# Optimization experiments

Measured on AMD Instinct MI355X. Metric: run time of the kernel, lower is better.

Reference implementation:

```python
import jax, jax.numpy as jnp
import numpy as np
from jax import lax

TOP_N = 4
CAT_NUM = 4
IOU_THRESH = 0.25
PAD = 224
OUT_SZ = 224


def _gen_edge_anchors():
    # Faithful port of NTSNet._generate_default_anchor_maps for 448x448 input.
    settings = (
        dict(stride=32, size=48, scale=[2 ** (1.0 / 3.0), 2 ** (2.0 / 3.0)], ar=[0.667, 1, 1.5]),
        dict(stride=64, size=96, scale=[2 ** (1.0 / 3.0), 2 ** (2.0 / 3.0)], ar=[0.667, 1, 1.5]),
        dict(stride=128, size=192, scale=[1, 2 ** (1.0 / 3.0), 2 ** (2.0 / 3.0)], ar=[0.667, 1, 1.5]),
    )
    inp = np.array([448, 448], dtype=np.float32)
    edges = []
    for s in settings:
        stride = s['stride']
        oh, ow = np.ceil(inp / stride).astype(int)
        ostart = stride / 2.0
        oy = np.arange(ostart, ostart + stride * oh, stride, dtype=np.float32).reshape(oh, 1)
        ox = np.arange(ostart, ostart + stride * ow, stride, dtype=np.float32).reshape(1, ow)
        cy = np.broadcast_to(oy, (oh, ow)); cx = np.broadcast_to(ox, (oh, ow))
        for sc in s['scale']:
            for ar in s['ar']:
                h = s['size'] * sc / float(ar) ** 0.5
                w = s['size'] * sc * float(ar) ** 0.5
                e = np.stack([cy - h / 2.0, cx - w / 2.0, cy + h / 2.0, cx + w / 2.0], axis=-1).reshape(-1, 4)
                edges.append(e)
    return np.concatenate(edges, 0).astype(np.float32)

EDGE_ANCHORS = (_gen_edge_anchors() + PAD).astype(np.int32)  # [1614,4] (y0,x0,y1,x1) in padded coords
BOXES_F = jnp.asarray(EDGE_ANCHORS, jnp.float32)
BOXES_I = jnp.asarray(EDGE_ANCHORS, jnp.int32)
AREAS = (BOXES_F[:, 2] - BOXES_F[:, 0]) * (BOXES_F[:, 3] - BOXES_F[:, 1])
N_ANCHORS = EDGE_ANCHORS.shape[0]  # 1614


def _nms_single(scores):
    # Greedy hard NMS: pick top score, suppress IoU >= thresh, repeat TOP_N times.
    def step(valid, _):
        s = jnp.where(valid, scores, -jnp.inf)
        i = jnp.argmax(s)
        b = BOXES_F[i]
        sy = jnp.maximum(BOXES_F[:, 0], b[0]); sx = jnp.maximum(BOXES_F[:, 1], b[1])
        ey = jnp.minimum(BOXES_F[:, 2], b[2]); ex = jnp.minimum(BOXES_F[:, 3], b[3])
        ly = ey - sy; lx = ex - sx
        inter = jnp.where((ly < 0) | (lx < 0), 0.0, ly * lx)
        iou = inter / (AREAS + AREAS[i] - inter)
        return valid & (iou < IOU_THRESH), i
    _, idx = lax.scan(step, jnp.ones((N_ANCHORS,), bool), None, length=TOP_N)
    return idx  # [TOP_N] int


def _crop_resize(img, box):
    # img: [3, 896, 896]; box: int [4] = (y0,x0,y1,x1); bilinear, align_corners=True -> [3,224,224]
    hmax = img.shape[-1] - 1
    y0, x0, y1, x1 = box[0], box[1], box[2], box[3]
    t = jnp.arange(OUT_SZ, dtype=jnp.float32) / (OUT_SZ - 1.0)
    ys = y0.astype(jnp.float32) + t * (y1 - y0 - 1).astype(jnp.float32)
    xs = x0.astype(jnp.float32) + t * (x1 - x0 - 1).astype(jnp.float32)
    yf = jnp.floor(ys); xf = jnp.floor(xs)
    wy = (ys - yf)[None, :, None]; wx = (xs - xf)[None, None, :]
    yl = yf.astype(jnp.int32); yh = jnp.minimum(yl + 1, hmax)
    xl = xf.astype(jnp.int32); xh = jnp.minimum(xl + 1, hmax)
    g = lambda yi, xi: img[:, yi[:, None], xi[None, :]]
    top = g(yl, xl) * (1.0 - wx) + g(yl, xh) * wx
    bot = g(yh, xl) * (1.0 - wx) + g(yh, xh) * wx
    return top * (1.0 - wy) + bot * wy


def _conv(x, w, b, stride, pad):
    y = lax.conv_general_dilated(x, w, (stride, stride), ((pad, pad), (pad, pad)),
                                 dimension_numbers=('NCHW', 'OIHW', 'NCHW'))
    return y + b[None, :, None, None]


def _forward(x, bb_w, bb_b, w1, b1, t1w, t1b, w2, b2, t2w, t2b, w3, b3, t3w, t3b, cw, cb):
    B = x.shape[0]
    backbone = lambda z: jax.nn.relu(_conv(z, bb_w, bb_b, 32, 0))
    raw_pre = backbone(x)  # [B,2048,14,14]
    # Navigator unit
    y1 = jax.nn.relu(_conv(raw_pre, w1, b1, 1, 1))                                  # [B,128,14,14]
    z1 = (jnp.einsum('bchw,oc->bohw', y1, t1w) + t1b[None, :, None, None]).reshape(B, -1)
    y2 = jax.nn.relu(_conv(y1, w2, b2, 2, 1))                                        # [B,128,7,7]
    z2 = (jnp.einsum('bchw,oc->bohw', y2, t2w) + t2b[None, :, None, None]).reshape(B, -1)
    y3 = jax.nn.relu(_conv(y2, w3, b3, 2, 1))                                        # [B,128,4,4]
    z3 = (jnp.einsum('bchw,oc->bohw', y3, t3w) + t3b[None, :, None, None]).reshape(B, -1)
    rpn_score = jnp.concatenate([z1, z2, z3], axis=1)  # [B,1614]
    top_idx = jax.vmap(_nms_single)(rpn_score)          # [B,TOP_N]
    boxes = BOXES_I[top_idx]                            # [B,TOP_N,4]
    x_pad = jnp.pad(x, ((0, 0), (0, 0), (PAD, PAD), (PAD, PAD)))  # [B,3,896,896]
    parts = jax.vmap(lambda img, bs: jax.vmap(lambda b: _crop_resize(img, b))(bs))(x_pad, boxes)
    parts = lax.stop_gradient(parts).reshape(B * TOP_N, 3, OUT_SZ, OUT_SZ)  # .detach() in torch
    part_feat = backbone(parts).mean(axis=(2, 3)).reshape(B, TOP_N, 2048)
    part_feat = part_feat[:, :CAT_NUM].reshape(B, -1)   # [B,8192]
    raw_feat = lax.stop_gradient(raw_pre).mean(axis=(2, 3))  # [B,2048] (detached in torch)
    concat = jnp.concatenate([part_feat, raw_feat], axis=1)  # [B,10240]
    return concat @ cw.T + cb                           # [B,200]


def setup_inputs() -> dict:
    key = jax.random.key(0)
    ks = jax.random.split(key, 12)
    def w(k, shape, fan_in):
        return jax.random.normal(k, shape, jnp.float32) * np.float32(np.sqrt(2.0 / fan_in))
    return {
        'x': jax.random.normal(ks[0], (8, 3, 448, 448), jnp.float32),
        'bb_w': w(ks[1], (2048, 3, 32, 32), 3 * 32 * 32), 'bb_b': jnp.zeros((2048,), jnp.float32),
        'w1': w(ks[2], (128, 2048, 3, 3), 2048 * 9), 'b1': jnp.zeros((128,), jnp.float32),
        't1w': w(ks[3], (6, 128), 128), 't1b': jnp.zeros((6,), jnp.float32),
        'w2': w(ks[4], (128, 128, 3, 3), 128 * 9), 'b2': jnp.zeros((128,), jnp.float32),
        't2w': w(ks[5], (6, 128), 128), 't2b': jnp.zeros((6,), jnp.float32),
        'w3': w(ks[6], (128, 128, 3, 3), 128 * 9), 'b3': jnp.zeros((128,), jnp.float32),
        't3w': w(ks[7], (9, 128), 128), 't3b': jnp.zeros((9,), jnp.float32),
        'cw': w(ks[8], (200, 2048 * (CAT_NUM + 1)), 2048 * (CAT_NUM + 1)),
        'cb': jnp.zeros((200,), jnp.float32),
    }


def reference(x, bb_w, bb_b, w1, b1, t1w, t1b, w2, b2, t2w, t2b, w3, b3, t3w, t3b, cw, cb):
    return _forward(x, bb_w, bb_b, w1, b1, t1w, t1b, w2, b2, t2w, t2b, w3, b3, t3w, t3b, cw, cb)
```

## Files before the change

### kernel.cpp

```cpp
#include <hip/hip_runtime.h>
#include <math.h>


typedef _Float16 h8 __attribute__((ext_vector_type(8)));
typedef float f32x4 __attribute__((ext_vector_type(4)));

#define ASCALE 256.0f
#define WSCALE 16384.0f
#define RSCALE (1.0f / (256.0f * 16384.0f))
#define PSLAB ((size_t)1664 * 2048)

__device__ __forceinline__ void gload16(const void* g, void* l) {
  __builtin_amdgcn_global_load_lds(
      (__attribute__((address_space(1))) void*)(void*)(uintptr_t)g,
      (__attribute__((address_space(3))) void*)l, 16, 0, 0);
}

__device__ void anchors_body(int i, int* anch, float* areas) {
  if (i >= 1614) return;
  int stride, oh, a, pos;
  double size, sc;
  const double C13 = 1.2599210498948732;
  const double C23 = 1.5874010519681994;
  if (i < 1176) {
    stride = 32; size = 48.0; oh = 14; a = i / 196; pos = i % 196;
    sc = (a / 3 == 0) ? C13 : C23;
  } else if (i < 1470) {
    int r = i - 1176; stride = 64; size = 96.0; oh = 7; a = r / 49; pos = r % 49;
    sc = (a / 3 == 0) ? C13 : C23;
  } else {
    int r = i - 1470; stride = 128; size = 192.0; oh = 4; a = r / 16; pos = r % 16;
    int si = a / 3;
    sc = (si == 0) ? 1.0 : ((si == 1) ? C13 : C23);
  }
  int ari = a % 3;
  double ar = (ari == 0) ? 0.667 : ((ari == 1) ? 1.0 : 1.5);
  int gy = pos / oh, gx = pos % oh;
  float cy = 0.5f * (float)stride + (float)(stride * gy);
  float cx = 0.5f * (float)stride + (float)(stride * gx);
  double ss = sqrt(ar);
  double hd = (size * sc) / ss;
  double wd = (size * sc) * ss;
  float hh = (float)(hd * 0.5), wh = (float)(wd * 0.5);
  int y0 = (int)((cy - hh) + 224.0f), x0 = (int)((cx - wh) + 224.0f);
  int y1i = (int)((cy + hh) + 224.0f), x1i = (int)((cx + wh) + 224.0f);
  anch[i * 4 + 0] = y0; anch[i * 4 + 1] = x0;
  anch[i * 4 + 2] = y1i; anch[i * 4 + 3] = x1i;
  areas[i] = (float)(y1i - y0) * (float)(x1i - x0);
}

__global__ __launch_bounds__(256) void prep_small(int* __restrict__ anch,
                                                  float* __restrict__ areas,
                                                  const float* __restrict__ w2,
                                                  float* __restrict__ w2p,
                                                  const float* __restrict__ w3,
                                                  float* __restrict__ w3p) {
  int b = blockIdx.x, t = threadIdx.x;
  if (b < 7) { anchors_body(b * 256 + t, anch, areas); return; }
  const float* src; float* dst; int idx;
  if (b < 7 + 576) { src = w2; dst = w2p; idx = (b - 7) * 256 + t; }
  else             { src = w3; dst = w3p; idx = (b - 583) * 256 + t; }
  if (idx >= 128 * 9 * 128) return;
  int c = idx % 128; int r2 = idx / 128; int tap = r2 % 9; int o = r2 / 9;
  dst[idx] = src[(o * 128 + c) * 9 + tap];
}

__global__ __launch_bounds__(256) void split_w(const float* __restrict__ src,
                                               _Float16* __restrict__ h,
                                               _Float16* __restrict__ l, int n8) {
  int i = blockIdx.x * 256 + threadIdx.x;
  if (i >= n8) return;
  float4 v0 = *(const float4*)(src + (size_t)i * 8);
  float4 v1 = *(const float4*)(src + (size_t)i * 8 + 4);
  float vv[8] = {v0.x, v0.y, v0.z, v0.w, v1.x, v1.y, v1.z, v1.w};
  h8 vh, vl;
#pragma unroll
  for (int j = 0; j < 8; ++j) {
    float s = vv[j] * WSCALE;
    _Float16 a = (_Float16)s;
    vh[j] = a; vl[j] = (_Float16)(s - (float)a);
  }
  *(h8*)(h + (size_t)i * 8) = vh;
  *(h8*)(l + (size_t)i * 8) = vl;
}

__global__ __launch_bounds__(256) void split_w1(const float* __restrict__ w1,
                                                _Float16* __restrict__ h,
                                                _Float16* __restrict__ l) {
  int idx = blockIdx.x * 256 + threadIdx.x;
  if (idx >= 128 * 9 * 2048) return;
  int c = idx & 2047; int rest = idx >> 11; int tap = rest % 9; int o = rest / 9;
  float v = w1[(o * 2048 + c) * 9 + tap] * WSCALE;
  _Float16 a = (_Float16)v;
  h[idx] = a; l[idx] = (_Float16)(v - (float)a);
}

__global__ __launch_bounds__(256) void split_x(const float* __restrict__ x,
                                               _Float16* __restrict__ Ah,
                                               _Float16* __restrict__ Al) {
  int i = blockIdx.x * 256 + threadIdx.x;
  if (i >= 1664 * 384) return;
  int kq = i % 384, m = i / 384;
  int k = kq * 8;
  h8 vh = {}, vl = {};
  if (m < 1568) {
    int b = m / 196, pos = m % 196;
    int c = k >> 10, r = (k >> 5) & 31, col = k & 31;
    int py = (pos / 14) * 32 + r, px = (pos % 14) * 32 + col;
    const float* sp2 = x + (((size_t)(b * 3 + c) * 448 + py) * 448 + px);
    float4 v0 = *(const float4*)sp2;
    float4 v1 = *(const float4*)(sp2 + 4);
    float vv[8] = {v0.x, v0.y, v0.z, v0.w, v1.x, v1.y, v1.z, v1.w};
#pragma unroll
    for (int j = 0; j < 8; ++j) {
      float s = vv[j] * ASCALE;
      _Float16 a = (_Float16)s;
      vh[j] = a; vl[j] = (_Float16)(s - (float)a);
    }
  }
  *(h8*)(Ah + (size_t)m * 3072 + k) = vh;
  *(h8*)(Al + (size_t)m * 3072 + k) = vl;
}

__global__ __launch_bounds__(256) void gemm_bb_mfma(
    const _Float16* __restrict__ Ah, const _Float16* __restrict__ Al,
    const _Float16* __restrict__ Bh, const _Float16* __restrict__ Bl,
    float* __restrict__ P) {
  __shared__ __align__(16) char lds[65536];
  const int t = threadIdx.x;
  const int bid = blockIdx.x + 13 * blockIdx.y;
  const int orig = (bid & 7) * 26 + (bid >> 3);
  const int m0 = (orig % 13) * 128, n0 = (orig / 13) * 128;
  const int kz = blockIdx.z;
  const int lane = t & 63, w = t >> 6;
  const int wm = (w >> 1) * 64, wn = (w & 1) * 64;
  const int lrow = lane & 15, kg = lane >> 4;

  int offA[4], offB[4];
#pragma unroll
  for (int i = 0; i < 4; ++i) {
    int ba = (wm + i * 16 + lrow) * 64 + kg * 16;
    offA[i] = ba ^ (((ba >> 7) & 3) << 4);
    int bb2 = (wn + i * 16 + lrow) * 64 + kg * 16;
    offB[i] = bb2 ^ (((bb2 >> 7) & 3) << 4);
  }
  size_t gAo[2], gBo[2];
  int ldso[2];
#pragma unroll
  for (int e = 0; e < 2; ++e) {
    int p = e * 256 + t;
    int lsl = p ^ ((p >> 3) & 3);
    int row = lsl >> 2, kq = lsl & 3;
    gAo[e] = (size_t)(m0 + row) * 3072 + kq * 8;
    gBo[e] = (size_t)(n0 + row) * 3072 + kq * 8;
    ldso[e] = e * 4096 + (t & 192) * 16;
  }

  auto STAGE = [&](int buf, int k0) {
    char* L = lds + buf * 32768;
#pragma unroll
    for (int e = 0; e < 2; ++e) {
      gload16(Ah + gAo[e] + k0, L + ldso[e]);
      gload16(Al + gAo[e] + k0, L + 8192 + ldso[e]);
      gload16(Bh + gBo[e] + k0, L + 16384 + ldso[e]);
      gload16(Bl + gBo[e] + k0, L + 24576 + ldso[e]);
    }
  };

  f32x4 acc[4][4] = {};
  const int kbeg = kz * 768, kend = kbeg + 768;
  STAGE(0, kbeg);
  __syncthreads();
  int cur = 0;
  for (int k0 = kbeg; k0 < kend; k0 += 32) {
    if (k0 + 32 < kend) STAGE(cur ^ 1, k0 + 32);
    const char* L = lds + cur * 32768;
    h8 fah[4], fal[4], fbh[4], fbl[4];
#pragma unroll
    for (int i = 0; i < 4; ++i) {
      fah[i] = *(const h8*)(L + offA[i]);
      fal[i] = *(const h8*)(L + 8192 + offA[i]);
      fbh[i] = *(const h8*)(L + 16384 + offB[i]);
      fbl[i] = *(const h8*)(L + 24576 + offB[i]);
    }
#pragma unroll
    for (int i = 0; i < 4; ++i)
#pragma unroll
      for (int j = 0; j < 4; ++j)
        acc[i][j] = __builtin_amdgcn_mfma_f32_16x16x32_f16(fah[i], fbh[j], acc[i][j], 0, 0, 0);
#pragma unroll
    for (int i = 0; i < 4; ++i)
#pragma unroll
      for (int j = 0; j < 4; ++j)
        acc[i][j] = __builtin_amdgcn_mfma_f32_16x16x32_f16(fah[i], fbl[j], acc[i][j], 0, 0, 0);
#pragma unroll
    for (int i = 0; i < 4; ++i)
#pragma unroll
      for (int j = 0; j < 4; ++j)
        acc[i][j] = __builtin_amdgcn_mfma_f32_16x16x32_f16(fal[i], fbh[j], acc[i][j], 0, 0, 0);
    __syncthreads();
    cur ^= 1;
  }
  float* Pz = P + (size_t)kz * PSLAB;
  const int prow = (lane >> 4) * 4;
#pragma unroll
  for (int i = 0; i < 4; ++i) {
#pragma unroll
    for (int j = 0; j < 4; ++j) {
      int n = n0 + wn + j * 16 + lrow;
#pragma unroll
      for (int r = 0; r < 4; ++r) {
        int m = m0 + wm + i * 16 + prow + r;
        Pz[(size_t)m * 2048 + n] = acc[i][j][r];
      }
    }
  }
}

template <int WRITE_SPLIT>
__global__ __launch_bounds__(256) void bb_reduce(const float* __restrict__ P,
                                                 const float* __restrict__ bias,
                                                 float* __restrict__ raw,
                                                 _Float16* __restrict__ h,
                                                 _Float16* __restrict__ l) {
  int idx = blockIdx.x * 256 + threadIdx.x;
  int m = idx >> 8, col = (idx & 255) * 8;
  if (WRITE_SPLIT) {
    if (m >= 1664) return;
    if (m >= 1568) {
      h8 z = {};
      *(h8*)(h + (size_t)m * 2048 + col) = z;
      *(h8*)(l + (size_t)m * 2048 + col) = z;
      return;
    }
  } else {
    if (m >= 1568) return;
  }
  size_t o = (size_t)m * 2048 + col;
  float v[8];
#pragma unroll
  for (int q = 0; q < 2; ++q) {
    float4 s0 = *(const float4*)(P + o + q * 4);
    float4 s1 = *(const float4*)(P + PSLAB + o + q * 4);
    float4 s2 = *(const float4*)(P + 2 * PSLAB + o + q * 4);
    float4 s3 = *(const float4*)(P + 3 * PSLAB + o + q * 4);
    float4 b = *(const float4*)(bias + col + q * 4);
    v[q * 4 + 0] = fmaxf(fmaf((s0.x + s1.x) + (s2.x + s3.x), RSCALE, b.x), 0.f);
    v[q * 4 + 1] = fmaxf(fmaf((s0.y + s1.y) + (s2.y + s3.y), RSCALE, b.y), 0.f);
    v[q * 4 + 2] = fmaxf(fmaf((s0.z + s1.z) + (s2.z + s3.z), RSCALE, b.z), 0.f);
    v[q * 4 + 3] = fmaxf(fmaf((s0.w + s1.w) + (s2.w + s3.w), RSCALE, b.w), 0.f);
  }
  *(float4*)(raw + o) = make_float4(v[0], v[1], v[2], v[3]);
  *(float4*)(raw + o + 4) = make_float4(v[4], v[5], v[6], v[7]);
  if (WRITE_SPLIT) {
    h8 vh, vl;
#pragma unroll
    for (int j = 0; j < 8; ++j) {
      float s = v[j] * ASCALE;
      _Float16 a = (_Float16)s;
      vh[j] = a; vl[j] = (_Float16)(s - (float)a);
    }
    *(h8*)(h + o) = vh;
    *(h8*)(l + o) = vl;
  }
}

__global__ __launch_bounds__(256) void gemm_nav_mfma(
    const _Float16* __restrict__ Ah, const _Float16* __restrict__ Al,
    const _Float16* __restrict__ Bh, const _Float16* __restrict__ Bl,
    float* __restrict__ part) {
  __shared__ __align__(16) char lds[65536];
  const int t = threadIdx.x;
  const int bid = blockIdx.x + 13 * blockIdx.y;
  const int orig = (bid & 7) * 52 + (bid >> 3);
  const int m0 = (orig % 13) * 128;
  const int sp = orig / 13;
  const int lane = t & 63, w = t >> 6;
  const int wm = (w >> 1) * 64, wn = (w & 1) * 64;
  const int lrow = lane & 15, kg = lane >> 4;

  int offA[4], offB[4];
#pragma unroll
  for (int i = 0; i < 4; ++i) {
    int ba = (wm + i * 16 + lrow) * 64 + kg * 16;
    offA[i] = ba ^ (((ba >> 7) & 3) << 4);
    int bb2 = (wn + i * 16 + lrow) * 64 + kg * 16;
    offB[i] = bb2 ^ (((bb2 >> 7) & 3) << 4);
  }
  size_t gBo[2];
  int ldso[2], akq8[2], ab[2], apy[2], apx[2], amv[2];
#pragma unroll
  for (int e = 0; e < 2; ++e) {
    int p = e * 256 + t;
    int lsl = p ^ ((p >> 3) & 3);
    int row = lsl >> 2, kq = lsl & 3;
    gBo[e] = (size_t)row * 18432 + kq * 8;
    ldso[e] = e * 4096 + (t & 192) * 16;
    int m = m0 + row;
    amv[e] = (m < 1568);
    int b = m / 196, pos = m % 196;
    ab[e] = b; apy[e] = pos / 14; apx[e] = pos % 14;
    akq8[e] = kq * 8;
  }

  auto STAGE = [&](int buf, int k0) {
    const int tap = k0 >> 11;
    const int c = k0 & 2047;
    const int dy = tap / 3 - 1, dx = tap % 3 - 1;
    char* L = lds + buf * 32768;
#pragma unroll
    for (int e = 0; e < 2; ++e) {
      int sy = apy[e] + dy, sx = apx[e] + dx;
      bool ok = amv[e] && ((unsigned)sy < 14u) && ((unsigned)sx < 14u);
      size_t rowi = ok ? (size_t)(ab[e] * 196 + sy * 14 + sx) : (size_t)1600;
      size_t ao = rowi * 2048 + c + akq8[e];
      gload16(Ah + ao, L + ldso[e]);
      gload16(Al + ao, L + 8192 + ldso[e]);
      gload16(Bh + gBo[e] + k0, L + 16384 + ldso[e]);
      gload16(Bl + gBo[e] + k0, L + 24576 + ldso[e]);
    }
  };

  f32x4 acc[4][4] = {};
  const int kbeg = sp * 576, kend = kbeg + 576;
  STAGE(0, kbeg);
  __syncthreads();
  int cur = 0;
  for (int k0 = kbeg; k0 < kend; k0 += 32) {
    if (k0 + 32 < kend) STAGE(cur ^ 1, k0 + 32);
    const char* L = lds + cur * 32768;
    h8 fah[4], fal[4], fbh[4], fbl[4];
#pragma unroll
    for (int i = 0; i < 4; ++i) {
      fah[i] = *(const h8*)(L + offA[i]);
      fal[i] = *(const h8*)(L + 8192 + offA[i]);
      fbh[i] = *(const h8*)(L + 16384 + offB[i]);
      fbl[i] = *(const h8*)(L + 24576 + offB[i]);
    }
#pragma unroll
    for (int i = 0; i < 4; ++i)
#pragma unroll
      for (int j = 0; j < 4; ++j)
        acc[i][j] = __builtin_amdgcn_mfma_f32_16x16x32_f16(fah[i], fbh[j], acc[i][j], 0, 0, 0);
#pragma unroll
    for (int i = 0; i < 4; ++i)
#pragma unroll
      for (int j = 0; j < 4; ++j)
        acc[i][j] = __builtin_amdgcn_mfma_f32_16x16x32_f16(fah[i], fbl[j], acc[i][j], 0, 0, 0);
#pragma unroll
    for (int i = 0; i < 4; ++i)
#pragma unroll
      for (int j = 0; j < 4; ++j)
        acc[i][j] = __builtin_amdgcn_mfma_f32_16x16x32_f16(fal[i], fbh[j], acc[i][j], 0, 0, 0);
    __syncthreads();
    cur ^= 1;
  }
  const int prow = (lane >> 4) * 4;
#pragma unroll
  for (int i = 0; i < 4; ++i) {
#pragma unroll
    for (int j = 0; j < 4; ++j) {
      int n = wn + j * 16 + lrow;
#pragma unroll
      for (int r = 0; r < 4; ++r) {
        int m = m0 + wm + i * 16 + prow + r;
        if (m < 1568)
          part[((size_t)sp * 1568 + m) * 128 + n] = acc[i][j][r] * RSCALE;
      }
    }
  }
}

__global__ __launch_bounds__(256) void y1_reduce(const float* __restrict__ part,
                                                 const float* __restrict__ b1,
                                                 float* __restrict__ y1) {
  int idx = blockIdx.x * 256 + threadIdx.x;
  if (idx >= 1568 * 128) return;
  int o = idx & 127;
  float s = b1[o];
#pragma unroll
  for (int sp = 0; sp < 32; ++sp) s += part[(size_t)sp * 1568 * 128 + idx];
  y1[idx] = fmaxf(s, 0.f);
}

__global__ __launch_bounds__(256) void conv3x3s2(const float* __restrict__ in,
                                                 const float* __restrict__ wp,
                                                 const float* __restrict__ bias,
                                                 float* __restrict__ out,
                                                 int Hin, int Hout) {
  int idx = blockIdx.x * 256 + threadIdx.x;
  int total = 8 * Hout * Hout * 128;
  if (idx >= total) return;
  int o = idx & 127; int pos = idx >> 7;
  int ox = pos % Hout; int t2 = pos / Hout; int oy = t2 % Hout; int b = t2 / Hout;
  float acc = bias[o];
  for (int dy = 0; dy < 3; ++dy) {
    int iy = 2 * oy - 1 + dy;
    if (iy < 0 || iy >= Hin) continue;
    for (int dx = 0; dx < 3; ++dx) {
      int ix = 2 * ox - 1 + dx;
      if (ix < 0 || ix >= Hin) continue;
      const float* ip = in + ((b * Hin + iy) * Hin + ix) * 128;
      const float* wgt = wp + (o * 9 + dy * 3 + dx) * 128;
#pragma unroll 4
      for (int c = 0; c < 128; c += 4) {
        float4 a = *(const float4*)(ip + c);
        float4 ww = *(const float4*)(wgt + c);
        acc += a.x * ww.x + a.y * ww.y + a.z * ww.z + a.w * ww.w;
      }
    }
  }
  out[idx] = fmaxf(acc, 0.f);
}

__global__ __launch_bounds__(256) void scores_kernel(
    const float* __restrict__ y1, const float* __restrict__ y2,
    const float* __restrict__ y3, const float* __restrict__ t1w,
    const float* __restrict__ t1b, const float* __restrict__ t2w,
    const float* __restrict__ t2b, const float* __restrict__ t3w,
    const float* __restrict__ t3b, float* __restrict__ scores) {
  int idx = blockIdx.x * 256 + threadIdx.x;
  if (idx >= 8 * 1614) return;
  int b = idx / 1614, sI = idx % 1614;
  const float* f; const float* w; float bias;
  if (sI < 1176) {
    int a = sI / 196;
    f = y1 + (b * 196 + (sI % 196)) * 128; w = t1w + a * 128; bias = t1b[a];
  } else if (sI < 1470) {
    int r = sI - 1176; int a = r / 49;
    f = y2 + (b * 49 + (r % 49)) * 128; w = t2w + a * 128; bias = t2b[a];
  } else {
    int r = sI - 1470; int a = r / 16;
    f = y3 + (b * 16 + (r % 16)) * 128; w = t3w + a * 128; bias = t3b[a];
  }
  float acc = 0.f;
  for (int c = 0; c < 128; c += 4) {
    float4 a4 = *(const float4*)(f + c);
    float4 w4 = *(const float4*)(w + c);
    acc += a4.x * w4.x + a4.y * w4.y + a4.z * w4.z + a4.w * w4.w;
  }
  scores[idx] = acc + bias;
}

__global__ __launch_bounds__(256) void nms_kernel(const float* __restrict__ scores,
                                                  const int* __restrict__ anch,
                                                  const float* __restrict__ areas,
                                                  int* __restrict__ boxes) {
  const int b = blockIdx.x, t = threadIdx.x;
  const float* s = scores + b * 1614;
  __shared__ unsigned char valid[1614];
  __shared__ float rv[256];
  __shared__ int ri[256];
  for (int i = t; i < 1614; i += 256) valid[i] = 1;
  __syncthreads();
  for (int n = 0; n < 4; ++n) {
    float best = -INFINITY; int bi = 0x7fffffff;
    for (int i = t; i < 1614; i += 256) {
      if (valid[i]) {
        float v = s[i];
        if (v > best || (v == best && i < bi)) { best = v; bi = i; }
      }
    }
    rv[t] = best; ri[t] = bi;
    __syncthreads();
    for (int off = 128; off > 0; off >>= 1) {
      if (t < off) {
        float ov = rv[t + off]; int oi = ri[t + off];
        if (ov > rv[t] || (ov == rv[t] && oi < ri[t])) { rv[t] = ov; ri[t] = oi; }
      }
      __syncthreads();
    }
    int sel = ri[0];
    if (sel > 1613) sel = 0;
    const int4 bb = ((const int4*)anch)[sel];
    const float Ai = areas[sel];
    if (t == 0) ((int4*)boxes)[b * 4 + n] = bb;
    __syncthreads();
    for (int i = t; i < 1614; i += 256) {
      if (!valid[i]) continue;
      const int4 ab = ((const int4*)anch)[i];
      float sy = fmaxf((float)ab.x, (float)bb.x);
      float sx = fmaxf((float)ab.y, (float)bb.y);
      float ey = fminf((float)ab.z, (float)bb.z);
      float ex = fminf((float)ab.w, (float)bb.w);
      float ly = ey - sy, lx = ex - sx;
      float inter = (ly < 0.f || lx < 0.f) ? 0.f : ly * lx;
      float iou = inter / (areas[i] + Ai - inter);
      if (iou >= 0.25f) valid[i] = 0;
    }
    __syncthreads();
  }
}

__global__ __launch_bounds__(256) void crop_kernel(const float* __restrict__ x,
                                                   const int* __restrict__ boxes,
                                                   _Float16* __restrict__ Ah,
                                                   _Float16* __restrict__ Al) {
  int idx = blockIdx.x * 256 + threadIdx.x;
  if (idx >= 32 * 3 * 224 * 224) return;
  int px = idx % 224; int t1 = idx / 224; int py = t1 % 224; int t2 = t1 / 224;
  int c = t2 % 3; int p = t2 / 3;
  int b = p >> 2;
  const int4 bb = ((const int4*)boxes)[p];
  float ty = (float)py / 223.0f;
  float txf = (float)px / 223.0f;
  float ys = (float)bb.x + ty * (float)(bb.z - bb.x - 1);
  float xs = (float)bb.y + txf * (float)(bb.w - bb.y - 1);
  float yf = floorf(ys), xf = floorf(xs);
  float wy = ys - yf, wx = xs - xf;
  int yl = (int)yf, xl = (int)xf;
  int yh = min(yl + 1, 895), xh = min(xl + 1, 895);
  const float* img = x + (size_t)(b * 3 + c) * 448 * 448;
  auto samp = [&](int yy, int xx) -> float {
    yy -= 224; xx -= 224;
    if (yy < 0 || yy >= 448 || xx < 0 || xx >= 448) return 0.f;
    return img[yy * 448 + xx];
  };
  float v00 = samp(yl, xl), v01 = samp(yl, xh);
  float v10 = samp(yh, xl), v11 = samp(yh, xh);
  float top = v00 * (1.f - wx) + v01 * wx;
  float bot = v10 * (1.f - wx) + v11 * wx;
  float val = top * (1.f - wy) + bot * wy;
  int i = py >> 5, r = py & 31, j = px >> 5, col = px & 31;
  int m = p * 49 + i * 7 + j;
  int k = (c << 10) + (r << 5) + col;
  float s = val * ASCALE;
  _Float16 a = (_Float16)s;
  Ah[(size_t)m * 3072 + k] = a;
  Al[(size_t)m * 3072 + k] = (_Float16)(s - (float)a);
}

__global__ __launch_bounds__(256) void mean_kernel(const float* __restrict__ in,
                                                   float* __restrict__ out,
                                                   int rows) {
  int g = blockIdx.x >> 5, chunk = blockIdx.x & 31;
  int col = chunk * 64 + (threadIdx.x & 63), rl = threadIdx.x >> 6;
  const float* base = in + ((size_t)g * rows) * 2048 + col;
  float s = 0.f;
  for (int r = rl; r < rows; r += 4) s += base[(size_t)r * 2048];
  __shared__ float red[4][64];
  red[rl][threadIdx.x & 63] = s;
  __syncthreads();
  if (rl == 0) {
    int c = threadIdx.x & 63;
    out[(size_t)g * 2048 + col] =
        ((red[0][c] + red[1][c]) + (red[2][c] + red[3][c])) / (float)rows;
  }
}

__global__ __launch_bounds__(256) void final_kernel(const float* __restrict__ pfeat,
                                                    const float* __restrict__ rfeat,
                                                    const float* __restrict__ cw,
                                                    const float* __restrict__ cb,
                                                    float* __restrict__ out) {
  int gw = (blockIdx.x * 256 + threadIdx.x) >> 6;
  int lane = threadIdx.x & 63;
  if (gw >= 1600) return;
  int b = gw / 200, j = gw % 200;
  const float* wr = cw + (size_t)j * 10240;
  const float* pf = pfeat + (size_t)b * 8192;
  float acc = 0.f;
  for (int k = lane * 4; k < 8192; k += 256) {
    float4 a = *(const float4*)(pf + k);
    float4 w = *(const float4*)(wr + k);
    acc += a.x * w.x + a.y * w.y + a.z * w.z + a.w * w.w;
  }
  const float* rf = rfeat + (size_t)b * 2048;
  const float* wr2 = wr + 8192;
  for (int k = lane * 4; k < 2048; k += 256) {
    float4 a = *(const float4*)(rf + k);
    float4 w = *(const float4*)(wr2 + k);
    acc += a.x * w.x + a.y * w.y + a.z * w.z + a.w * w.w;
  }
#pragma unroll
  for (int off = 32; off > 0; off >>= 1) acc += __shfl_down(acc, off, 64);
  if (lane == 0) out[b * 200 + j] = acc + cb[j];
}

extern "C" void kernel_launch(void* const* d_in, const int* in_sizes, int n_in,
                              void* d_out, int out_size, void* d_ws, size_t ws_size,
                              hipStream_t stream) {
  const float* x   = (const float*)d_in[0];
  const float* bbw = (const float*)d_in[1];
  const float* bbb = (const float*)d_in[2];
  const float* w1  = (const float*)d_in[3];
  const float* b1  = (const float*)d_in[4];
  const float* t1w = (const float*)d_in[5];
  const float* t1b = (const float*)d_in[6];
  const float* w2  = (const float*)d_in[7];
  const float* b2  = (const float*)d_in[8];
  const float* t2w = (const float*)d_in[9];
  const float* t2b = (const float*)d_in[10];
  const float* w3  = (const float*)d_in[11];
  const float* b3  = (const float*)d_in[12];
  const float* t3w = (const float*)d_in[13];
  const float* t3b = (const float*)d_in[14];
  const float* cw  = (const float*)d_in[15];
  const float* cb  = (const float*)d_in[16];
  float* out = (float*)d_out;

  char* p = (char*)d_ws;
  auto alloc = [&](size_t bytes) -> char* {
    char* r = p; p += (bytes + 255) & ~(size_t)255; return r;
  };
  int*      anch  = (int*)     alloc((size_t)1614 * 4 * 4);
  float*    areas = (float*)   alloc((size_t)1614 * 4);
  _Float16* bWh   = (_Float16*)alloc((size_t)2048 * 3072 * 2);
  _Float16* bWl   = (_Float16*)alloc((size_t)2048 * 3072 * 2);
  _Float16* w1h   = (_Float16*)alloc((size_t)128 * 18432 * 2);
  _Float16* w1l   = (_Float16*)alloc((size_t)128 * 18432 * 2);
  _Float16* Ahh   = (_Float16*)alloc((size_t)1664 * 3072 * 2);
  _Float16* All   = (_Float16*)alloc((size_t)1664 * 3072 * 2);
  _Float16* rawh  = (_Float16*)alloc((size_t)1664 * 2048 * 2);
  _Float16* rawl  = (_Float16*)alloc((size_t)1664 * 2048 * 2);
  float*    raw   = (float*)   alloc((size_t)1568 * 2048 * 4);
  float*    w2p   = (float*)   alloc((size_t)128 * 9 * 128 * 4);
  float*    w3p   = (float*)   alloc((size_t)128 * 9 * 128 * 4);
  char*     big   = alloc((size_t)4 * PSLAB * 4);
  float*    Pbuf  = (float*)big;
  float*    y1s   = (float*)big;
  float*    y1v   = (float*)   alloc((size_t)1568 * 128 * 4);
  float*    y2v   = (float*)   alloc((size_t)392 * 128 * 4);
  float*    y3v   = (float*)   alloc((size_t)128 * 128 * 4);
  float*    sc    = (float*)   alloc((size_t)8 * 1614 * 4);
  int*      boxes = (int*)     alloc((size_t)8 * 4 * 4 * 4);
  float*    pfeat = (float*)   alloc((size_t)32 * 2048 * 4);
  float*    rfeat = (float*)   alloc((size_t)8 * 2048 * 4);

  prep_small<<<7 + 576 + 576, 256, 0, stream>>>(anch, areas, w2, w2p, w3, w3p);
  split_w<<<(2048 * 3072 / 8 + 255) / 256, 256, 0, stream>>>(bbw, bWh, bWl, 2048 * 3072 / 8);
  split_w1<<<(128 * 9 * 2048 + 255) / 256, 256, 0, stream>>>(w1, w1h, w1l);
  split_x<<<(1664 * 384 + 255) / 256, 256, 0, stream>>>(x, Ahh, All);

  gemm_bb_mfma<<<dim3(13, 16, 4), 256, 0, stream>>>(Ahh, All, bWh, bWl, Pbuf);
  bb_reduce<1><<<1664, 256, 0, stream>>>(Pbuf, bbb, raw, rawh, rawl);
  gemm_nav_mfma<<<dim3(13, 32), 256, 0, stream>>>(rawh, rawl, w1h, w1l, y1s);
  y1_reduce<<<(1568 * 128 + 255) / 256, 256, 0, stream>>>(y1s, b1, y1v);
  mean_kernel<<<8 * 32, 256, 0, stream>>>(raw, rfeat, 196);
  conv3x3s2<<<(8 * 7 * 7 * 128 + 255) / 256, 256, 0, stream>>>(y1v, w2p, b2, y2v, 14, 7);
  conv3x3s2<<<(8 * 4 * 4 * 128 + 255) / 256, 256, 0, stream>>>(y2v, w3p, b3, y3v, 7, 4);
  scores_kernel<<<(8 * 1614 + 255) / 256, 256, 0, stream>>>(
      y1v, y2v, y3v, t1w, t1b, t2w, t2b, t3w, t3b, sc);
  nms_kernel<<<8, 256, 0, stream>>>(sc, anch, areas, boxes);
  crop_kernel<<<(32 * 3 * 224 * 224) / 256, 256, 0, stream>>>(x, boxes, Ahh, All);
  gemm_bb_mfma<<<dim3(13, 16, 4), 256, 0, stream>>>(Ahh, All, bWh, bWl, Pbuf);
  bb_reduce<0><<<1568, 256, 0, stream>>>(Pbuf, bbb, raw, rawh, rawl);
  mean_kernel<<<32 * 32, 256, 0, stream>>>(raw, pfeat, 49);
  final_kernel<<<400, 256, 0, stream>>>(pfeat, rfeat, cw, cb, out);
}
```

Measured before the change: 392.3 us.

## Load A fragments directly from global memory, halve LDS to raise occupancy

In both MFMA GEMM kernels, the A operand (hi/lo fp16 splits) is no longer staged through LDS. Each wave now loads its A fragments straight from global memory into registers every k-step, and only B stays double-buffered in LDS. This halves LDS use to 32 KB and sets launch bounds to 3 blocks per CU, aiming for more occupancy and fewer LDS writes and reads. The cost is that A rows shared by the two N-waves are fetched twice from global or cache, and the loads are synchronous with no prefetch, so their latency sits in the loop before the MFMAs.

```diff
diff --git a/kernel.cpp b/kernel.cpp
--- a/kernel.cpp
+++ b/kernel.cpp
@@ -122,11 +122,11 @@
   *(h8*)(Al + (size_t)m * 3072 + k) = vl;
 }
 
-__global__ __launch_bounds__(256) void gemm_bb_mfma(
+__global__ __launch_bounds__(256, 3) void gemm_bb_mfma(
     const _Float16* __restrict__ Ah, const _Float16* __restrict__ Al,
     const _Float16* __restrict__ Bh, const _Float16* __restrict__ Bl,
     float* __restrict__ P) {
-  __shared__ __align__(16) char lds[65536];
+  __shared__ __align__(16) char lds[32768];
   const int t = threadIdx.x;
   const int bid = blockIdx.x + 13 * blockIdx.y;
   const int orig = (bid & 7) * 26 + (bid >> 3);
@@ -134,36 +134,36 @@
   const int kz = blockIdx.z;
   const int lane = t & 63, w = t >> 6;
   const int wm = (w >> 1) * 64, wn = (w & 1) * 64;
-  const int lrow = lane & 15, kg = lane >> 4;
-
-  int offA[4], offB[4];
+  const int lrow = lane & 15, kg = lane >> 4, kg8 = kg * 8;
+
+  int offB[4];
 #pragma unroll
   for (int i = 0; i < 4; ++i) {
-    int ba = (wm + i * 16 + lrow) * 64 + kg * 16;
-    offA[i] = ba ^ (((ba >> 7) & 3) << 4);
     int bb2 = (wn + i * 16 + lrow) * 64 + kg * 16;
     offB[i] = bb2 ^ (((bb2 >> 7) & 3) << 4);
   }
-  size_t gAo[2], gBo[2];
+  size_t aro[4];
+#pragma unroll
+  for (int i = 0; i < 4; ++i)
+    aro[i] = (size_t)(m0 + wm + i * 16 + lrow) * 3072 + kg8;
+
+  size_t gBo[2];
   int ldso[2];
 #pragma unroll
   for (int e = 0; e < 2; ++e) {
     int p = e * 256 + t;
     int lsl = p ^ ((p >> 3) & 3);
     int row = lsl >> 2, kq = lsl & 3;
-    gAo[e] = (size_t)(m0 + row) * 3072 + kq * 8;
     gBo[e] = (size_t)(n0 + row) * 3072 + kq * 8;
     ldso[e] = e * 4096 + (t & 192) * 16;
   }
 
   auto STAGE = [&](int buf, int k0) {
-    char* L = lds + buf * 32768;
+    char* L = lds + buf * 16384;
 #pragma unroll
     for (int e = 0; e < 2; ++e) {
-      gload16(Ah + gAo[e] + k0, L + ldso[e]);
-      gload16(Al + gAo[e] + k0, L + 8192 + ldso[e]);
-      gload16(Bh + gBo[e] + k0, L + 16384 + ldso[e]);
-      gload16(Bl + gBo[e] + k0, L + 24576 + ldso[e]);
+      gload16(Bh + gBo[e] + k0, L + ldso[e]);
+      gload16(Bl + gBo[e] + k0, L + 8192 + ldso[e]);
     }
   };
 
@@ -173,15 +173,19 @@
   __syncthreads();
   int cur = 0;
   for (int k0 = kbeg; k0 < kend; k0 += 32) {
+    h8 fah[4], fal[4];
+#pragma unroll
+    for (int i = 0; i < 4; ++i) {
+      fah[i] = *(const h8*)(Ah + aro[i] + k0);
+      fal[i] = *(const h8*)(Al + aro[i] + k0);
+    }
     if (k0 + 32 < kend) STAGE(cur ^ 1, k0 + 32);
-    const char* L = lds + cur * 32768;
-    h8 fah[4], fal[4], fbh[4], fbl[4];
-#pragma unroll
-    for (int i = 0; i < 4; ++i) {
-      fah[i] = *(const h8*)(L + offA[i]);
-      fal[i] = *(const h8*)(L + 8192 + offA[i]);
-      fbh[i] = *(const h8*)(L + 16384 + offB[i]);
-      fbl[i] = *(const h8*)(L + 24576 + offB[i]);
+    const char* L = lds + cur * 16384;
+    h8 fbh[4], fbl[4];
+#pragma unroll
+    for (int j = 0; j < 4; ++j) {
+      fbh[j] = *(const h8*)(L + offB[j]);
+      fbl[j] = *(const h8*)(L + 8192 + offB[j]);
     }
 #pragma unroll
     for (int i = 0; i < 4; ++i)
@@ -265,11 +269,11 @@
   }
 }
 
-__global__ __launch_bounds__(256) void gemm_nav_mfma(
+__global__ __launch_bounds__(256, 3) void gemm_nav_mfma(
     const _Float16* __restrict__ Ah, const _Float16* __restrict__ Al,
     const _Float16* __restrict__ Bh, const _Float16* __restrict__ Bl,
     float* __restrict__ part) {
-  __shared__ __align__(16) char lds[65536];
+  __shared__ __align__(16) char lds[32768];
   const int t = threadIdx.x;
   const int bid = blockIdx.x + 13 * blockIdx.y;
   const int orig = (bid & 7) * 52 + (bid >> 3);
@@ -277,18 +281,25 @@
   const int sp = orig / 13;
   const int lane = t & 63, w = t >> 6;
   const int wm = (w >> 1) * 64, wn = (w & 1) * 64;
-  const int lrow = lane & 15, kg = lane >> 4;
-
-  int offA[4], offB[4];
+  const int lrow = lane & 15, kg = lane >> 4, kg8 = kg * 8;
+
+  int offB[4];
 #pragma unroll
   for (int i = 0; i < 4; ++i) {
-    int ba = (wm + i * 16 + lrow) * 64 + kg * 16;
-    offA[i] = ba ^ (((ba >> 7) & 3) << 4);
     int bb2 = (wn + i * 16 + lrow) * 64 + kg * 16;
     offB[i] = bb2 ^ (((bb2 >> 7) & 3) << 4);
   }
+  int fb[4], fpy[4], fpx[4], fvalid[4];
+#pragma unroll
+  for (int i = 0; i < 4; ++i) {
+    int m = m0 + wm + i * 16 + lrow;
+    fvalid[i] = (m < 1568);
+    int b = m / 196, pos = m % 196;
+    fb[i] = b; fpy[i] = pos / 14; fpx[i] = pos % 14;
+  }
+
   size_t gBo[2];
-  int ldso[2], akq8[2], ab[2], apy[2], apx[2], amv[2];
+  int ldso[2];
 #pragma unroll
   for (int e = 0; e < 2; ++e) {
     int p = e * 256 + t;
@@ -296,28 +307,14 @@
     int row = lsl >> 2, kq = lsl & 3;
     gBo[e] = (size_t)row * 18432 + kq * 8;
     ldso[e] = e * 4096 + (t & 192) * 16;
-    int m = m0 + row;
-    amv[e] = (m < 1568);
-    int b = m / 196, pos = m % 196;
-    ab[e] = b; apy[e] = pos / 14; apx[e] = pos % 14;
-    akq8[e] = kq * 8;
   }
 
   auto STAGE = [&](int buf, int k0) {
-    const int tap = k0 >> 11;
-    const int c = k0 & 2047;
-    const int dy = tap / 3 - 1, dx = tap % 3 - 1;
-    char* L = lds + buf * 32768;
+    char* L = lds + buf * 16384;
 #pragma unroll
     for (int e = 0; e < 2; ++e) {
-      int sy = apy[e] + dy, sx = apx[e] + dx;
-      bool ok = amv[e] && ((unsigned)sy < 14u) && ((unsigned)sx < 14u);
-      size_t rowi = ok ? (size_t)(ab[e] * 196 + sy * 14 + sx) : (size_t)1600;
-      size_t ao = rowi * 2048 + c + akq8[e];
-      gload16(Ah + ao, L + ldso[e]);
-      gload16(Al + ao, L + 8192 + ldso[e]);
-      gload16(Bh + gBo[e] + k0, L + 16384 + ldso[e]);
-      gload16(Bl + gBo[e] + k0, L + 24576 + ldso[e]);
+      gload16(Bh + gBo[e] + k0, L + ldso[e]);
+      gload16(Bl + gBo[e] + k0, L + 8192 + ldso[e]);
     }
   };
 
@@ -327,15 +324,26 @@
   __syncthreads();
   int cur = 0;
   for (int k0 = kbeg; k0 < kend; k0 += 32) {
+    const int tap = k0 >> 11;
+    const int c = k0 & 2047;
+    const int dy = tap / 3 - 1, dx = tap % 3 - 1;
+    h8 fah[4], fal[4];
+#pragma unroll
+    for (int i = 0; i < 4; ++i) {
+      int sy = fpy[i] + dy, sx = fpx[i] + dx;
+      bool ok = fvalid[i] && ((unsigned)sy < 14u) && ((unsigned)sx < 14u);
+      size_t rowi = ok ? (size_t)(fb[i] * 196 + sy * 14 + sx) : (size_t)1600;
+      size_t ao = rowi * 2048 + c + kg8;
+      fah[i] = *(const h8*)(Ah + ao);
+      fal[i] = *(const h8*)(Al + ao);
+    }
     if (k0 + 32 < kend) STAGE(cur ^ 1, k0 + 32);
-    const char* L = lds + cur * 32768;
-    h8 fah[4], fal[4], fbh[4], fbl[4];
-#pragma unroll
-    for (int i = 0; i < 4; ++i) {
-      fah[i] = *(const h8*)(L + offA[i]);
-      fal[i] = *(const h8*)(L + 8192 + offA[i]);
-      fbh[i] = *(const h8*)(L + 16384 + offB[i]);
-      fbl[i] = *(const h8*)(L + 24576 + offB[i]);
+    const char* L = lds + cur * 16384;
+    h8 fbh[4], fbl[4];
+#pragma unroll
+    for (int j = 0; j < 4; ++j) {
+      fbh[j] = *(const h8*)(L + offB[j]);
+      fbl[j] = *(const h8*)(L + 8192 + offB[j]);
     }
 #pragma unroll
     for (int i = 0; i < 4; ++i)
```

New measurement: 509.3 us. 29.8% more time.

## Halve backbone split-K and fuse bias/ReLU/mean into partial-sum reduction

Applied to the files above, without the earlier changes.

The backbone GEMM split-K factor drops from 4 to 2, so each block covers twice the K range and half as many partial slabs are written and read back. The separate fp32 raw activation buffer and mean kernel are removed. A new feat_reduce kernel sums the two partial slabs, applies bias and ReLU, and averages rows directly, while the split-hi/lo producer writes only the fp16 halves. The second backbone pass no longer runs an elementwise reduce at all. The cost is fewer GEMM blocks in flight, so occupancy on the GPU is lower, and the partial slabs are read twice by the two reduce kernels after the first pass.

```diff
diff --git a/kernel.cpp b/kernel.cpp
--- a/kernel.cpp
+++ b/kernel.cpp
@@ -168,7 +168,7 @@
   };
 
   f32x4 acc[4][4] = {};
-  const int kbeg = kz * 768, kend = kbeg + 768;
+  const int kbeg = kz * 1536, kend = kbeg + 1536;
   STAGE(0, kbeg);
   __syncthreads();
   int cur = 0;
@@ -217,51 +217,61 @@
   }
 }
 
-template <int WRITE_SPLIT>
-__global__ __launch_bounds__(256) void bb_reduce(const float* __restrict__ P,
-                                                 const float* __restrict__ bias,
-                                                 float* __restrict__ raw,
-                                                 _Float16* __restrict__ h,
-                                                 _Float16* __restrict__ l) {
+__global__ __launch_bounds__(256) void bb_reduce_split(const float* __restrict__ P,
+                                                       const float* __restrict__ bias,
+                                                       _Float16* __restrict__ h,
+                                                       _Float16* __restrict__ l) {
   int idx = blockIdx.x * 256 + threadIdx.x;
   int m = idx >> 8, col = (idx & 255) * 8;
-  if (WRITE_SPLIT) {
-    if (m >= 1664) return;
-    if (m >= 1568) {
-      h8 z = {};
-      *(h8*)(h + (size_t)m * 2048 + col) = z;
-      *(h8*)(l + (size_t)m * 2048 + col) = z;
-      return;
-    }
-  } else {
-    if (m >= 1568) return;
-  }
+  if (m >= 1664) return;
   size_t o = (size_t)m * 2048 + col;
-  float v[8];
+  if (m >= 1568) {
+    h8 z = {};
+    *(h8*)(h + o) = z;
+    *(h8*)(l + o) = z;
+    return;
+  }
+  h8 vh, vl;
 #pragma unroll
   for (int q = 0; q < 2; ++q) {
     float4 s0 = *(const float4*)(P + o + q * 4);
     float4 s1 = *(const float4*)(P + PSLAB + o + q * 4);
-    float4 s2 = *(const float4*)(P + 2 * PSLAB + o + q * 4);
-    float4 s3 = *(const float4*)(P + 3 * PSLAB + o + q * 4);
     float4 b = *(const float4*)(bias + col + q * 4);
-    v[q * 4 + 0] = fmaxf(fmaf((s0.x + s1.x) + (s2.x + s3.x), RSCALE, b.x), 0.f);
-    v[q * 4 + 1] = fmaxf(fmaf((s0.y + s1.y) + (s2.y + s3.y), RSCALE, b.y), 0.f);
-    v[q * 4 + 2] = fmaxf(fmaf((s0.z + s1.z) + (s2.z + s3.z), RSCALE, b.z), 0.f);
-    v[q * 4 + 3] = fmaxf(fmaf((s0.w + s1.w) + (s2.w + s3.w), RSCALE, b.w), 0.f);
-  }
-  *(float4*)(raw + o) = make_float4(v[0], v[1], v[2], v[3]);
-  *(float4*)(raw + o + 4) = make_float4(v[4], v[5], v[6], v[7]);
-  if (WRITE_SPLIT) {
-    h8 vh, vl;
-#pragma unroll
-    for (int j = 0; j < 8; ++j) {
+    float v[4];
+    v[0] = fmaxf(fmaf(s0.x + s1.x, RSCALE, b.x), 0.f);
+    v[1] = fmaxf(fmaf(s0.y + s1.y, RSCALE, b.y), 0.f);
+    v[2] = fmaxf(fmaf(s0.z + s1.z, RSCALE, b.z), 0.f);
+    v[3] = fmaxf(fmaf(s0.w + s1.w, RSCALE, b.w), 0.f);
+#pragma unroll
+    for (int j = 0; j < 4; ++j) {
       float s = v[j] * ASCALE;
       _Float16 a = (_Float16)s;
-      vh[j] = a; vl[j] = (_Float16)(s - (float)a);
-    }
-    *(h8*)(h + o) = vh;
-    *(h8*)(l + o) = vl;
+      vh[q * 4 + j] = a; vl[q * 4 + j] = (_Float16)(s - (float)a);
+    }
+  }
+  *(h8*)(h + o) = vh;
+  *(h8*)(l + o) = vl;
+}
+
+__global__ __launch_bounds__(256) void feat_reduce(const float* __restrict__ P,
+                                                   const float* __restrict__ bias,
+                                                   float* __restrict__ out,
+                                                   int rows) {
+  int g = blockIdx.x >> 5, chunk = blockIdx.x & 31;
+  int col = chunk * 64 + (threadIdx.x & 63), rl = threadIdx.x >> 6;
+  const float* base0 = P + ((size_t)g * rows) * 2048 + col;
+  const float* base1 = base0 + PSLAB;
+  float bcol = bias[col];
+  float s = 0.f;
+  for (int r = rl; r < rows; r += 4)
+    s += fmaxf(fmaf(base0[(size_t)r * 2048] + base1[(size_t)r * 2048], RSCALE, bcol), 0.f);
+  __shared__ float red[4][64];
+  red[rl][threadIdx.x & 63] = s;
+  __syncthreads();
+  if (rl == 0) {
+    int c = threadIdx.x & 63;
+    out[(size_t)g * 2048 + col] =
+        ((red[0][c] + red[1][c]) + (red[2][c] + red[3][c])) / (float)rows;
   }
 }
 
@@ -530,24 +540,6 @@
   Al[(size_t)m * 3072 + k] = (_Float16)(s - (float)a);
 }
 
-__global__ __launch_bounds__(256) void mean_kernel(const float* __restrict__ in,
-                                                   float* __restrict__ out,
-                                                   int rows) {
-  int g = blockIdx.x >> 5, chunk = blockIdx.x & 31;
-  int col = chunk * 64 + (threadIdx.x & 63), rl = threadIdx.x >> 6;
-  const float* base = in + ((size_t)g * rows) * 2048 + col;
-  float s = 0.f;
-  for (int r = rl; r < rows; r += 4) s += base[(size_t)r * 2048];
-  __shared__ float red[4][64];
-  red[rl][threadIdx.x & 63] = s;
-  __syncthreads();
-  if (rl == 0) {
-    int c = threadIdx.x & 63;
-    out[(size_t)g * 2048 + col] =
-        ((red[0][c] + red[1][c]) + (red[2][c] + red[3][c])) / (float)rows;
-  }
-}
-
 __global__ __launch_bounds__(256) void final_kernel(const float* __restrict__ pfeat,
                                                     const float* __restrict__ rfeat,
                                                     const float* __restrict__ cw,
@@ -613,10 +605,9 @@
   _Float16* All   = (_Float16*)alloc((size_t)1664 * 3072 * 2);
   _Float16* rawh  = (_Float16*)alloc((size_t)1664 * 2048 * 2);
   _Float16* rawl  = (_Float16*)alloc((size_t)1664 * 2048 * 2);
-  float*    raw   = (float*)   alloc((size_t)1568 * 2048 * 4);
   float*    w2p   = (float*)   alloc((size_t)128 * 9 * 128 * 4);
   float*    w3p   = (float*)   alloc((size_t)128 * 9 * 128 * 4);
-  char*     big   = alloc((size_t)4 * PSLAB * 4);
+  char*     big   = alloc((size_t)2 * PSLAB * 4);
   float*    Pbuf  = (float*)big;
   float*    y1s   = (float*)big;
   float*    y1v   = (float*)   alloc((size_t)1568 * 128 * 4);
@@ -632,19 +623,18 @@
   split_w1<<<(128 * 9 * 2048 + 255) / 256, 256, 0, stream>>>(w1, w1h, w1l);
   split_x<<<(1664 * 384 + 255) / 256, 256, 0, stream>>>(x, Ahh, All);
 
-  gemm_bb_mfma<<<dim3(13, 16, 4), 256, 0, stream>>>(Ahh, All, bWh, bWl, Pbuf);
-  bb_reduce<1><<<1664, 256, 0, stream>>>(Pbuf, bbb, raw, rawh, rawl);
+  gemm_bb_mfma<<<dim3(13, 16, 2), 256, 0, stream>>>(Ahh, All, bWh, bWl, Pbuf);
+  bb_reduce_split<<<1664, 256, 0, stream>>>(Pbuf, bbb, rawh, rawl);
+  feat_reduce<<<8 * 32, 256, 0, stream>>>(Pbuf, bbb, rfeat, 196);
   gemm_nav_mfma<<<dim3(13, 32), 256, 0, stream>>>(rawh, rawl, w1h, w1l, y1s);
   y1_reduce<<<(1568 * 128 + 255) / 256, 256, 0, stream>>>(y1s, b1, y1v);
-  mean_kernel<<<8 * 32, 256, 0, stream>>>(raw, rfeat, 196);
   conv3x3s2<<<(8 * 7 * 7 * 128 + 255) / 256, 256, 0, stream>>>(y1v, w2p, b2, y2v, 14, 7);
   conv3x3s2<<<(8 * 4 * 4 * 128 + 255) / 256, 256, 0, stream>>>(y2v, w3p, b3, y3v, 7, 4);
   scores_kernel<<<(8 * 1614 + 255) / 256, 256, 0, stream>>>(
       y1v, y2v, y3v, t1w, t1b, t2w, t2b, t3w, t3b, sc);
   nms_kernel<<<8, 256, 0, stream>>>(sc, anch, areas, boxes);
   crop_kernel<<<(32 * 3 * 224 * 224) / 256, 256, 0, stream>>>(x, boxes, Ahh, All);
-  gemm_bb_mfma<<<dim3(13, 16, 4), 256, 0, stream>>>(Ahh, All, bWh, bWl, Pbuf);
-  bb_reduce<0><<<1568, 256, 0, stream>>>(Pbuf, bbb, raw, rawh, rawl);
-  mean_kernel<<<32 * 32, 256, 0, stream>>>(raw, pfeat, 49);
+  gemm_bb_mfma<<<dim3(13, 16, 2), 256, 0, stream>>>(Ahh, All, bWh, bWl, Pbuf);
+  feat_reduce<<<32 * 32, 256, 0, stream>>>(Pbuf, bbb, pfeat, 49);
   final_kernel<<<400, 256, 0, stream>>>(pfeat, rfeat, cw, cb, out);
 }
```

New measurement: 372.9 us. 1.05x faster.
